# Performance work log

Hardware: AMD Instinct MI355X
Metric: run time of the kernel (lower is better)

Reference implementation:

```python
import jax, jax.numpy as jnp
import numpy as np


def setup_inputs() -> dict:
    key = jax.random.key(0)
    k1, k2, k3, k4 = jax.random.split(key, 4)
    H, B, S = 1024, 32, 4096
    hidden = jax.random.normal(k1, (1, B, H), dtype=jnp.float32)
    encoder_outputs = jax.random.normal(k2, (S, B, H), dtype=jnp.float32)
    attn_W = jax.random.normal(k3, (H, H), dtype=jnp.float32) * (1.0 / np.sqrt(H))
    attn_b = jax.random.normal(k4, (H,), dtype=jnp.float32) * 0.01
    return {"hidden": hidden, "encoder_outputs": encoder_outputs,
            "attn_W": attn_W, "attn_b": attn_b}


def reference(hidden, encoder_outputs, attn_W, attn_b):
    # method == 'general':
    #   energy[b, i] = hidden[0, b] . (attn_W @ encoder_outputs[i, b] + attn_b)
    # Linear: enc @ W.T + b, applied over [S, B, H]
    proj = jnp.einsum('sbh,gh->sbg', encoder_outputs, attn_W) + attn_b  # [S, B, H]
    energies = jnp.einsum('bh,sbh->bs', hidden[0], proj)               # [B, S]
    # F.softmax on 2D defaults to last dim (seq dim), then unsqueeze(1)
    normalized = jax.nn.softmax(energies, axis=-1)[:, None, :]         # [B, 1, S]
    return normalized
```

## Files before the change

### kernel.cpp

```cpp
#include <hip/hip_runtime.h>
#include <math.h>

constexpr int H = 1024;
constexpr int B = 32;
constexpr int S = 4096;
constexpr int STILE = 64;

__global__ __launch_bounds__(256) void compute_v_kernel(
    const float* __restrict__ hidden, const float* __restrict__ W,
    float* __restrict__ v)
{
    const int b  = blockIdx.x >> 4;
    const int hc = blockIdx.x & 15;
    const int hq = threadIdx.x & 15;
    const int gg = threadIdx.x >> 4;
    const int hquad = hc * 16 + hq;
    const float* __restrict__ hb = hidden + b * H;
    const float4* __restrict__ W4 = (const float4*)W;

    float4 aE = {0,0,0,0}, aO = {0,0,0,0};
    const int g0 = gg * 64;
    #pragma unroll 4
    for (int g = g0; g < g0 + 64; g += 2) {
        float  h0 = hb[g], h1 = hb[g + 1];
        float4 w0 = W4[(size_t)(g + 0) * 256 + hquad];
        float4 w1 = W4[(size_t)(g + 1) * 256 + hquad];
        aE.x = fmaf(h0, w0.x, aE.x); aE.y = fmaf(h0, w0.y, aE.y);
        aE.z = fmaf(h0, w0.z, aE.z); aE.w = fmaf(h0, w0.w, aE.w);
        aO.x = fmaf(h1, w1.x, aO.x); aO.y = fmaf(h1, w1.y, aO.y);
        aO.z = fmaf(h1, w1.z, aO.z); aO.w = fmaf(h1, w1.w, aO.w);
    }
    float4 acc = {aE.x + aO.x, aE.y + aO.y, aE.z + aO.z, aE.w + aO.w};

    __shared__ float4 part[16][16];
    part[gg][hq] = acc;
    __syncthreads();
    if (threadIdx.x < 64) {
        const int q  = threadIdx.x & 15;
        const int kk = threadIdx.x >> 4;
        float4 s = part[kk * 4 + 0][q];
        #pragma unroll
        for (int j = 1; j < 4; ++j) {
            float4 p = part[kk * 4 + j][q];
            s.x += p.x; s.y += p.y; s.z += p.z; s.w += p.w;
        }
        part[kk * 4][q] = s;
    }
    __syncthreads();
    if (threadIdx.x < 16) {
        const int q = threadIdx.x;
        float4 s = part[0][q];
        #pragma unroll
        for (int j = 1; j < 4; ++j) {
            float4 p = part[j * 4][q];
            s.x += p.x; s.y += p.y; s.z += p.z; s.w += p.w;
        }
        ((float4*)(v + b * H))[hquad] = s;
    }
}

__global__ __launch_bounds__(256) void energies_kernel(
    const float* __restrict__ enc, const float* __restrict__ v,
    float* __restrict__ energies)
{
    const int b  = blockIdx.x & 31;
    const int s0 = (blockIdx.x >> 5) * STILE;

    __shared__ float4 vs[H / 4];
    const float4* __restrict__ vb = (const float4*)(v + b * H);
    for (int i = threadIdx.x; i < H / 4; i += 256) vs[i] = vb[i];
    __syncthreads();

    const int wave = threadIdx.x >> 6;
    const int lane = threadIdx.x & 63;

    for (int si = wave; si < STILE; si += 4) {
        const int s = s0 + si;
        const float4* __restrict__ row =
            (const float4*)(enc + ((size_t)s * B + b) * H);
        float acc = 0.f;
        #pragma unroll
        for (int it = 0; it < 4; ++it) {
            float4 e = row[it * 64 + lane];
            float4 w = vs[it * 64 + lane];
            acc = fmaf(e.x, w.x, acc);
            acc = fmaf(e.y, w.y, acc);
            acc = fmaf(e.z, w.z, acc);
            acc = fmaf(e.w, w.w, acc);
        }
        #pragma unroll
        for (int off = 32; off > 0; off >>= 1)
            acc += __shfl_xor(acc, off, 64);
        if (lane == 0) energies[b * S + s] = acc;
    }
}

__global__ __launch_bounds__(256) void softmax_kernel(float* __restrict__ out)
{
    const int b = blockIdx.x;
    float* __restrict__ row = out + (size_t)b * S;
    __shared__ float redm[4];
    __shared__ float reds[4];
    const int wave = threadIdx.x >> 6;
    const int lane = threadIdx.x & 63;

    float vals[S / 256];
    float m = -INFINITY;
    #pragma unroll
    for (int k = 0; k < S / 256; ++k) {
        vals[k] = row[threadIdx.x + k * 256];
        m = fmaxf(m, vals[k]);
    }
    #pragma unroll
    for (int off = 32; off > 0; off >>= 1)
        m = fmaxf(m, __shfl_xor(m, off, 64));
    if (lane == 0) redm[wave] = m;
    __syncthreads();
    m = fmaxf(fmaxf(redm[0], redm[1]), fmaxf(redm[2], redm[3]));

    float ssum = 0.f;
    #pragma unroll
    for (int k = 0; k < S / 256; ++k) {
        vals[k] = __expf(vals[k] - m);
        ssum += vals[k];
    }
    #pragma unroll
    for (int off = 32; off > 0; off >>= 1)
        ssum += __shfl_xor(ssum, off, 64);
    if (lane == 0) reds[wave] = ssum;
    __syncthreads();
    const float inv = 1.0f / ((reds[0] + reds[1]) + (reds[2] + reds[3]));
    #pragma unroll
    for (int k = 0; k < S / 256; ++k)
        row[threadIdx.x + k * 256] = vals[k] * inv;
}

extern "C" void kernel_launch(void* const* d_in, const int* in_sizes, int n_in,
                              void* d_out, int out_size, void* d_ws, size_t ws_size,
                              hipStream_t stream) {
    const float* hidden = (const float*)d_in[0];
    const float* enc    = (const float*)d_in[1];
    const float* W      = (const float*)d_in[2];
    float* out = (float*)d_out;
    float* v   = (float*)d_ws;

    compute_v_kernel<<<dim3(B * 16), dim3(256), 0, stream>>>(hidden, W, v);
    energies_kernel<<<dim3(B * (S / STILE)), dim3(256), 0, stream>>>(enc, v, out);
    softmax_kernel<<<dim3(B), dim3(256), 0, stream>>>(out);
}
```

Measured before the change: 131.5 us.

## Restructure energies kernel into contiguous-chunk blocks with register-resident v vectors

The energies kernel now runs 256 blocks of 1024 threads. Each block reads a contiguous 512-row slab of the encoder outputs. Each wave holds the v vectors for two batch indices in registers instead of staging one batch's v in shared memory, and it processes two rows per iteration using split accumulators. The aim is to make the streaming read of the 512 MB encoder tensor fully sequential per block and to give each wave more loads in flight, while removing the shared-memory load and its barrier. The risks are lower occupancy from the 1024-thread blocks and register pressure, plus a launch of only 256 blocks.

Measured after the change: 112.2 us. 14.7% less time.

```diff
diff --git a/kernel.cpp b/kernel.cpp
--- a/kernel.cpp
+++ b/kernel.cpp
@@ -4,7 +4,6 @@
 constexpr int H = 1024;
 constexpr int B = 32;
 constexpr int S = 4096;
-constexpr int STILE = 64;
 
 __global__ __launch_bounds__(256) void compute_v_kernel(
     const float* __restrict__ hidden, const float* __restrict__ W,
@@ -59,39 +58,59 @@
     }
 }
 
-__global__ __launch_bounds__(256) void energies_kernel(
+__global__ __launch_bounds__(1024) void energies_kernel(
     const float* __restrict__ enc, const float* __restrict__ v,
     float* __restrict__ energies)
 {
-    const int b  = blockIdx.x & 31;
-    const int s0 = (blockIdx.x >> 5) * STILE;
+    const int w    = threadIdx.x >> 6;
+    const int lane = threadIdx.x & 63;
+    const int b0 = w, b1 = w + 16;
+    const size_t base   = (size_t)blockIdx.x * 512;
+    const int    s_base = blockIdx.x * 16;
 
-    __shared__ float4 vs[H / 4];
-    const float4* __restrict__ vb = (const float4*)(v + b * H);
-    for (int i = threadIdx.x; i < H / 4; i += 256) vs[i] = vb[i];
-    __syncthreads();
+    const float4* __restrict__ v4 = (const float4*)v;
+    const float4 wa0 = v4[b0 * 256 + lane],       wa1 = v4[b0 * 256 + 64 + lane],
+                 wa2 = v4[b0 * 256 + 128 + lane], wa3 = v4[b0 * 256 + 192 + lane];
+    const float4 wb0 = v4[b1 * 256 + lane],       wb1 = v4[b1 * 256 + 64 + lane],
+                 wb2 = v4[b1 * 256 + 128 + lane], wb3 = v4[b1 * 256 + 192 + lane];
 
-    const int wave = threadIdx.x >> 6;
-    const int lane = threadIdx.x & 63;
+    for (int k = 0; k < 16; ++k) {
+        const float4* __restrict__ rowA =
+            (const float4*)enc + (base + (size_t)w + 32u * k) * 256;
+        const float4* __restrict__ rowB = rowA + 16 * 256;
+        float4 a0 = rowA[lane],       a1 = rowA[64 + lane],
+               a2 = rowA[128 + lane], a3 = rowA[192 + lane];
+        float4 e0 = rowB[lane],       e1 = rowB[64 + lane],
+               e2 = rowB[128 + lane], e3 = rowB[192 + lane];
 
-    for (int si = wave; si < STILE; si += 4) {
-        const int s = s0 + si;
-        const float4* __restrict__ row =
-            (const float4*)(enc + ((size_t)s * B + b) * H);
-        float acc = 0.f;
+        float pa0 = a0.x * wa0.x, pa1 = a1.x * wa1.x;
+        float pb0 = e0.x * wb0.x, pb1 = e1.x * wb1.x;
+        pa0 = fmaf(a0.y, wa0.y, pa0); pa1 = fmaf(a1.y, wa1.y, pa1);
+        pb0 = fmaf(e0.y, wb0.y, pb0); pb1 = fmaf(e1.y, wb1.y, pb1);
+        pa0 = fmaf(a0.z, wa0.z, pa0); pa1 = fmaf(a1.z, wa1.z, pa1);
+        pb0 = fmaf(e0.z, wb0.z, pb0); pb1 = fmaf(e1.z, wb1.z, pb1);
+        pa0 = fmaf(a0.w, wa0.w, pa0); pa1 = fmaf(a1.w, wa1.w, pa1);
+        pb0 = fmaf(e0.w, wb0.w, pb0); pb1 = fmaf(e1.w, wb1.w, pb1);
+        pa0 = fmaf(a2.x, wa2.x, pa0); pa1 = fmaf(a3.x, wa3.x, pa1);
+        pb0 = fmaf(e2.x, wb2.x, pb0); pb1 = fmaf(e3.x, wb3.x, pb1);
+        pa0 = fmaf(a2.y, wa2.y, pa0); pa1 = fmaf(a3.y, wa3.y, pa1);
+        pb0 = fmaf(e2.y, wb2.y, pb0); pb1 = fmaf(e3.y, wb3.y, pb1);
+        pa0 = fmaf(a2.z, wa2.z, pa0); pa1 = fmaf(a3.z, wa3.z, pa1);
+        pb0 = fmaf(e2.z, wb2.z, pb0); pb1 = fmaf(e3.z, wb3.z, pb1);
+        pa0 = fmaf(a2.w, wa2.w, pa0); pa1 = fmaf(a3.w, wa3.w, pa1);
+        pb0 = fmaf(e2.w, wb2.w, pb0); pb1 = fmaf(e3.w, wb3.w, pb1);
+        float pa = pa0 + pa1;
+        float pb = pb0 + pb1;
+
         #pragma unroll
-        for (int it = 0; it < 4; ++it) {
-            float4 e = row[it * 64 + lane];
-            float4 w = vs[it * 64 + lane];
-            acc = fmaf(e.x, w.x, acc);
-            acc = fmaf(e.y, w.y, acc);
-            acc = fmaf(e.z, w.z, acc);
-            acc = fmaf(e.w, w.w, acc);
+        for (int off = 32; off > 0; off >>= 1) {
+            pa += __shfl_xor(pa, off, 64);
+            pb += __shfl_xor(pb, off, 64);
         }
-        #pragma unroll
-        for (int off = 32; off > 0; off >>= 1)
-            acc += __shfl_xor(acc, off, 64);
-        if (lane == 0) energies[b * S + s] = acc;
+        if (lane == 0) {
+            energies[(size_t)b0 * S + s_base + k] = pa;
+            energies[(size_t)b1 * S + s_base + k] = pb;
+        }
     }
 }
 
@@ -145,6 +164,6 @@
     float* v   = (float*)d_ws;
 
     compute_v_kernel<<<dim3(B * 16), dim3(256), 0, stream>>>(hidden, W, v);
-    energies_kernel<<<dim3(B * (S / STILE)), dim3(256), 0, stream>>>(enc, v, out);
+    energies_kernel<<<dim3(256), dim3(1024), 0, stream>>>(enc, v, out);
     softmax_kernel<<<dim3(B), dim3(256), 0, stream>>>(out);
 }
```
